# Kernel optimization log

Hardware: AMD Instinct MI355X
Metric: run time of the kernel (lower is better)

The kernel has to match this reference:

```python
import jax, jax.numpy as jnp
import numpy as np

B, C, T, F = 4, 2, 4224, 256
L = 256          # sequence_len (block size over time)
STRIDE = 128
H = 8            # num_heads
RF = L // 2      # receptive_field default


def setup_inputs() -> dict:
    key = jax.random.key(0)
    k0, k1, k2, k3, k4 = jax.random.split(key, 5)
    s = 0.05
    return {
        "x": jax.random.normal(k0, (B, C, T, F), dtype=jnp.float32),
        "w_in": jax.random.normal(k1, (3 * F, F), dtype=jnp.float32) * s,
        "b_in": jax.random.normal(k2, (3 * F,), dtype=jnp.float32) * s,
        "w_out": jax.random.normal(k3, (F, F), dtype=jnp.float32) * s,
        "b_out": jax.random.normal(k4, (F,), dtype=jnp.float32) * s,
    }


def reference(x, w_in, b_in, w_out, b_out):
    b, c, t, f = x.shape
    nb = (t - L) // STRIDE + 1              # num_blocks
    dh = f // H                              # head dim

    # --- UnfoldSpectrogram: (B,C,T,F) -> (B,C,nb,L,F) ---
    idx = jnp.arange(nb)[:, None] * STRIDE + jnp.arange(L)[None, :]  # (nb, L)
    blocks = x[:, :, idx, :]                 # (B,C,nb,L,F)

    # --- MultiheadAttention over flattened batch of blocks ---
    xb = blocks.reshape(b * c * nb, L, f)    # (N,L,F)
    qkv = xb @ w_in.T + b_in                 # (N,L,3F)
    q, k, v = jnp.split(qkv, 3, axis=-1)
    q = q.reshape(-1, L, H, dh)
    k = k.reshape(-1, L, H, dh)
    v = v.reshape(-1, L, H, dh)

    scale = 1.0 / np.sqrt(dh).astype(np.float32)
    scores = jnp.einsum("nihd,njhd->nhij", q, k) * scale  # (N,H,L,L)

    # Faithful to the original: the Longformer mask is a FLOAT 0/1 tensor that
    # torch's MultiheadAttention ADDS to the scores (band gets +1.0).
    di = jnp.arange(L)[:, None] - jnp.arange(L)[None, :]
    band = ((di >= 0) & (di < RF)).astype(scores.dtype)   # (L,L)
    scores = scores + band

    attn = jax.nn.softmax(scores, axis=-1)
    o = jnp.einsum("nhij,njhd->nihd", attn, v).reshape(-1, L, f)
    o = o @ w_out.T + b_out                  # (N,L,F)

    # --- FoldSpectrogram: overlap-add then normalize by overlap count ---
    ob = o.reshape(b, c, nb, L, f)
    y = jnp.zeros((b, c, t, f), dtype=o.dtype).at[:, :, idx, :].add(ob)
    cnt = jnp.zeros((t,), dtype=o.dtype).at[idx.reshape(-1)].add(1.0)
    return y / cnt[None, None, :, None]
```

## Files before the change

### kernel.cpp

```cpp
#include <hip/hip_runtime.h>

typedef unsigned short u16;
typedef unsigned int u32;
typedef __attribute__((ext_vector_type(8))) short bf16x8;
typedef __attribute__((ext_vector_type(4))) float f32x4;
typedef __attribute__((ext_vector_type(4))) u32 u32x4;
typedef __attribute__((ext_vector_type(2))) u32 u32x2;

__device__ __forceinline__ u16 f2bf(float f) {
  u32 u = __builtin_bit_cast(u32, f);
  return (u16)((u + 0x7FFFu + ((u >> 16) & 1u)) >> 16);
}
__device__ __forceinline__ float bf2f(u16 b) {
  return __builtin_bit_cast(float, (u32)b << 16);
}

__device__ __forceinline__ u32 cvtpk(float lo, float hi) {
  u32 r;
  asm("v_cvt_pk_bf16_f32 %0, %1, %2" : "=v"(r) : "v"(lo), "v"(hi));
  return r;
}

__device__ __forceinline__ float fexp2(float x) {
#if __has_builtin(__builtin_amdgcn_exp2f)
  return __builtin_amdgcn_exp2f(x);
#else
  return __expf(x * 0.6931471805599453f);
#endif
}

__device__ __forceinline__ void lds_async16(const void* g, void* l) {
  auto gp = reinterpret_cast<const __attribute__((address_space(1))) u32*>(
      reinterpret_cast<uintptr_t>(g));
  auto lp = reinterpret_cast<__attribute__((address_space(3))) u32*>(
      reinterpret_cast<uintptr_t>(l));
  __builtin_amdgcn_global_load_lds(gp, lp, 16, 0, 0);
}

__global__ void cvt2_kernel(const float* __restrict__ a, const float* __restrict__ b,
                            u16* __restrict__ oa, u16* __restrict__ ob, int na4, int nb4) {
  int i = blockIdx.x * 256 + threadIdx.x;
  const float* src;
  u16* dst;
  int idx;
  if (i < na4) {
    src = a; dst = oa; idx = i;
  } else {
    idx = i - na4;
    if (idx >= nb4) return;
    src = b; dst = ob;
  }
  f32x4 v = *(const f32x4*)(src + (size_t)idx * 4);
  u32x2 o;
  o[0] = (u32)f2bf(v[0]) | ((u32)f2bf(v[1]) << 16);
  o[1] = (u32)f2bf(v[2]) | ((u32)f2bf(v[3]) << 16);
  *(u32x2*)(dst + (size_t)idx * 4) = o;
}

template <bool OUT_BF16, bool A_F32>
__global__ __launch_bounds__(256) void gemm_bt_kernel(
    const void* __restrict__ A, const u16* __restrict__ B,
    const float* __restrict__ bias, void* __restrict__ C,
    int M, int N, int K) {
  __shared__ u16 sA[128 * 32];
  __shared__ u16 sB[128 * 32];
  const int tid = threadIdx.x;
  const int m0 = blockIdx.x * 128;
  const int n0 = blockIdx.y * 128;
  const int w = tid >> 6;
  const int lane = tid & 63;
  const int wr = (w >> 1) * 64;
  const int wc = (w & 1) * 64;
  const int lm = lane & 15;
  const int lk = (lane >> 4) * 8;

  f32x4 acc[4][4] = {};

  const int srow = tid >> 2;
  const int ssub = (tid & 3) * 8;
  const u16* Ag = (const u16*)A + (size_t)(m0 + srow) * K + ssub;
  const float* Agf = (const float*)A + (size_t)(m0 + srow) * K + ssub;
  const u16* Bg = B + (size_t)(n0 + srow) * K + ssub;
  const size_t rstep = (size_t)64 * K;

  for (int k0 = 0; k0 < K; k0 += 32) {
    f32x4 a00, a01, a10, a11;
    if constexpr (A_F32) {
      a00 = *(const f32x4*)(Agf + k0);
      a01 = *(const f32x4*)(Agf + k0 + 4);
      a10 = *(const f32x4*)(Agf + rstep + k0);
      a11 = *(const f32x4*)(Agf + rstep + k0 + 4);
    }
    __syncthreads();
    if constexpr (A_F32) {
      u32x4 w0, w1;
      w0[0] = cvtpk(a00[0], a00[1]); w0[1] = cvtpk(a00[2], a00[3]);
      w0[2] = cvtpk(a01[0], a01[1]); w0[3] = cvtpk(a01[2], a01[3]);
      w1[0] = cvtpk(a10[0], a10[1]); w1[1] = cvtpk(a10[2], a10[3]);
      w1[2] = cvtpk(a11[0], a11[1]); w1[3] = cvtpk(a11[2], a11[3]);
      *(u32x4*)&sA[tid * 8] = w0;
      *(u32x4*)&sA[2048 + tid * 8] = w1;
    } else {
      lds_async16(Ag + k0, &sA[tid * 8]);
      lds_async16(Ag + rstep + k0, &sA[2048 + tid * 8]);
    }
    lds_async16(Bg + k0, &sB[tid * 8]);
    lds_async16(Bg + rstep + k0, &sB[2048 + tid * 8]);
    __syncthreads();
    bf16x8 af[4], bfr[4];
#pragma unroll
    for (int i = 0; i < 4; ++i)
      af[i] = *(const bf16x8*)&sA[(wr + i * 16 + lm) * 32 + lk];
#pragma unroll
    for (int j = 0; j < 4; ++j)
      bfr[j] = *(const bf16x8*)&sB[(wc + j * 16 + lm) * 32 + lk];
#pragma unroll
    for (int i = 0; i < 4; ++i)
#pragma unroll
      for (int j = 0; j < 4; ++j)
        acc[i][j] = __builtin_amdgcn_mfma_f32_16x16x32_bf16(af[i], bfr[j], acc[i][j], 0, 0, 0);
  }

  const int r0 = (lane >> 4) * 4;
#pragma unroll
  for (int j = 0; j < 4; ++j) {
    const int n = n0 + wc + j * 16 + lm;
    const float bv = bias[n];
#pragma unroll
    for (int i = 0; i < 4; ++i) {
#pragma unroll
      for (int r = 0; r < 4; ++r) {
        const int m = m0 + wr + i * 16 + r0 + r;
        float v = acc[i][j][r] + bv;
        if (OUT_BF16)
          ((u16*)C)[(size_t)m * N + n] = f2bf(v);
        else
          ((float*)C)[(size_t)m * N + n] = v;
      }
    }
  }
}

__global__ __launch_bounds__(256, 2) void attn_kernel(const u16* __restrict__ qkv,
                                                      u16* __restrict__ o_ws) {
  __shared__ u16 sVt[32 * 264];
  __shared__ u16 sP[4 * 32 * 40];

  const int bid = blockIdx.x;
  const int n = bid >> 3;
  const int h = bid & 7;
  const int rowbase = (n >> 5) * 4224 + (n & 31) * 128;
  const int tid = threadIdx.x;
  const int w = tid >> 6;
  const int lane = tid & 63;
  const int lm = lane & 15;
  const int lg = lane >> 4;

#pragma unroll
  for (int it = 0; it < 4; ++it) {
    int c = it * 256 + tid;
    int row = c >> 2;
    int sub = (c & 3) * 8;
    int rsw = row ^ ((sub >> 3) << 4);
    const u16* gv = qkv + (size_t)(rowbase + row) * 768 + 512 + h * 32 + sub;
    u32x4 vv = *(const u32x4*)gv;
#pragma unroll
    for (int q = 0; q < 4; ++q) {
      sVt[(sub + 2 * q) * 264 + rsw] = (u16)(vv[q] & 0xFFFFu);
      sVt[(sub + 2 * q + 1) * 264 + rsw] = (u16)(vv[q] >> 16);
    }
  }

  bf16x8 qf[4];
#pragma unroll
  for (int rt = 0; rt < 4; ++rt) {
    int row = rowbase + w * 64 + rt * 16 + lm;
    qf[rt] = *(const bf16x8*)(qkv + (size_t)row * 768 + h * 32 + lg * 8);
  }

  const u16* kbase = qkv + (size_t)(rowbase + lm) * 768 + 256 + h * 32 + lg * 8;

  bf16x8 kfc[2];
#pragma unroll
  for (int ct = 0; ct < 2; ++ct)
    kfc[ct] = *(const bf16x8*)(kbase + (size_t)(ct * 16) * 768);

  __syncthreads();

  f32x4 oacc[4][2] = {};
  f32x4 lacc[4] = {};
  u16* myP = sP + w * (32 * 40);
  const float C1 = 0.25500035370494726f;
  const float C2 = 1.4426950408889634f;
  const int jq = lg * 4;
  const int D0w = w * 64;
  const bf16x8 onesb = {(short)0x3F80, (short)0x3F80, (short)0x3F80, (short)0x3F80,
                        (short)0x3F80, (short)0x3F80, (short)0x3F80, (short)0x3F80};

#pragma unroll 1
  for (int ch = 0; ch < 8; ++ch) {
    const int chn = (ch < 7) ? ch + 1 : 7;
    bf16x8 kfn[2], vf[2];
#pragma unroll
    for (int ct = 0; ct < 2; ++ct)
      kfn[ct] = *(const bf16x8*)(kbase + (size_t)(chn * 32 + ct * 16) * 768);
#pragma unroll
    for (int ctd = 0; ctd < 2; ++ctd) {
      int d = ctd * 16 + lm;
      vf[ctd] = *(const bf16x8*)&sVt[d * 264 + ((ch * 32 + lg * 8) ^ ((d >> 3) << 4))];
    }

#pragma unroll
    for (int hf = 0; hf < 2; ++hf) {
#pragma unroll
      for (int ct = 0; ct < 2; ++ct) {
#pragma unroll
        for (int rl = 0; rl < 2; ++rl) {
          const int rt = hf * 2 + rl;
          f32x4 s = __builtin_amdgcn_mfma_f32_16x16x32_bf16(kfc[ct], qf[rt], f32x4{0.f, 0.f, 0.f, 0.f}, 0, 0, 0);
          const int D0 = D0w + rt * 16 - (ch * 32 + ct * 16);
          float p0, p1, p2, p3;
          if (D0 >= 16 && D0 <= 112) {
            p0 = fexp2(__builtin_fmaf(s[0], C1, C2));
            p1 = fexp2(__builtin_fmaf(s[1], C1, C2));
            p2 = fexp2(__builtin_fmaf(s[2], C1, C2));
            p3 = fexp2(__builtin_fmaf(s[3], C1, C2));
          } else if (D0 == 0) {
            p0 = fexp2(__builtin_fmaf(s[0], C1, (lm >= jq + 0) ? C2 : 0.0f));
            p1 = fexp2(__builtin_fmaf(s[1], C1, (lm >= jq + 1) ? C2 : 0.0f));
            p2 = fexp2(__builtin_fmaf(s[2], C1, (lm >= jq + 2) ? C2 : 0.0f));
            p3 = fexp2(__builtin_fmaf(s[3], C1, (lm >= jq + 3) ? C2 : 0.0f));
          } else if (D0 == 128) {
            p0 = fexp2(__builtin_fmaf(s[0], C1, (lm < jq + 0) ? C2 : 0.0f));
            p1 = fexp2(__builtin_fmaf(s[1], C1, (lm < jq + 1) ? C2 : 0.0f));
            p2 = fexp2(__builtin_fmaf(s[2], C1, (lm < jq + 2) ? C2 : 0.0f));
            p3 = fexp2(__builtin_fmaf(s[3], C1, (lm < jq + 3) ? C2 : 0.0f));
          } else {
            p0 = fexp2(s[0] * C1);
            p1 = fexp2(s[1] * C1);
            p2 = fexp2(s[2] * C1);
            p3 = fexp2(s[3] * C1);
          }
          u32 a0, a1;
          asm("v_cvt_pk_bf16_f32 %0, %1, %2" : "=v"(a0) : "v"(p0), "v"(p1));
          asm("v_cvt_pk_bf16_f32 %0, %1, %2" : "=v"(a1) : "v"(p2), "v"(p3));
          u32x2 pk;
          pk[0] = a0;
          pk[1] = a1;
          *(u32x2*)&myP[(rl * 16 + lm) * 40 + ct * 16 + jq] = pk;
        }
      }
      bf16x8 pf[2];
#pragma unroll
      for (int rl = 0; rl < 2; ++rl)
        pf[rl] = *(const bf16x8*)&myP[(rl * 16 + lm) * 40 + lg * 8];
      __asm__ __volatile__("" ::: "memory");
      __builtin_amdgcn_s_setprio(1);
#pragma unroll
      for (int rl = 0; rl < 2; ++rl) {
        lacc[hf * 2 + rl] =
            __builtin_amdgcn_mfma_f32_16x16x32_bf16(pf[rl], onesb, lacc[hf * 2 + rl], 0, 0, 0);
#pragma unroll
        for (int ctd = 0; ctd < 2; ++ctd)
          oacc[hf * 2 + rl][ctd] =
              __builtin_amdgcn_mfma_f32_16x16x32_bf16(pf[rl], vf[ctd], oacc[hf * 2 + rl][ctd], 0, 0, 0);
      }
      __builtin_amdgcn_s_setprio(0);
    }
    kfc[0] = kfn[0];
    kfc[1] = kfn[1];
  }

#pragma unroll
  for (int rt = 0; rt < 4; ++rt) {
#pragma unroll
    for (int r = 0; r < 4; ++r) {
      float inv = 1.0f / lacc[rt][r];
      int i_g = w * 64 + rt * 16 + jq + r;
#pragma unroll
      for (int ctd = 0; ctd < 2; ++ctd) {
        float v = oacc[rt][ctd][r] * inv;
        u32 u = __builtin_bit_cast(u32, v) + 0x8000u;
        o_ws[((size_t)(n * 256 + i_g)) * 256 + h * 32 + ctd * 16 + lm] = (u16)(u >> 16);
      }
    }
  }
}

__global__ void combine_kernel(const u16* __restrict__ o_ws, u16* __restrict__ oc) {
  int gid = blockIdx.x * 256 + threadIdx.x;
  int m = gid >> 5;
  int f0 = (gid & 31) << 3;
  int bc = m / 4224;
  int t = m - bc * 4224;
  int i0 = t >> 7;
  float a[8] = {0.f, 0.f, 0.f, 0.f, 0.f, 0.f, 0.f, 0.f};
  if (i0 <= 31) {
    const u16* p = o_ws + ((size_t)((bc * 32 + i0) * 256 + (t - (i0 << 7)))) * 256 + f0;
    u32x4 v = *(const u32x4*)p;
#pragma unroll
    for (int q = 0; q < 4; ++q) {
      a[2 * q] += bf2f((u16)(v[q] & 0xFFFFu));
      a[2 * q + 1] += bf2f((u16)(v[q] >> 16));
    }
  }
  if (i0 >= 1) {
    int i1 = i0 - 1;
    const u16* p = o_ws + ((size_t)((bc * 32 + i1) * 256 + (t - (i1 << 7)))) * 256 + f0;
    u32x4 v = *(const u32x4*)p;
#pragma unroll
    for (int q = 0; q < 4; ++q) {
      a[2 * q] += bf2f((u16)(v[q] & 0xFFFFu));
      a[2 * q + 1] += bf2f((u16)(v[q] >> 16));
    }
  }
  float sc = (i0 >= 1 && i0 <= 31) ? 0.5f : 1.0f;
  u32x2 o;
  o[0] = (u32)f2bf(a[0] * sc) | ((u32)f2bf(a[1] * sc) << 16);
  o[1] = (u32)f2bf(a[2] * sc) | ((u32)f2bf(a[3] * sc) << 16);
  u32x2 o2;
  o2[0] = (u32)f2bf(a[4] * sc) | ((u32)f2bf(a[5] * sc) << 16);
  o2[1] = (u32)f2bf(a[6] * sc) | ((u32)f2bf(a[7] * sc) << 16);
  u16* dst = oc + (size_t)m * 256 + f0;
  *(u32x2*)dst = o;
  *(u32x2*)(dst + 4) = o2;
}

extern "C" void kernel_launch(void* const* d_in, const int* in_sizes, int n_in,
                              void* d_out, int out_size, void* d_ws, size_t ws_size,
                              hipStream_t stream) {
  const float* x = (const float*)d_in[0];
  const float* w_in = (const float*)d_in[1];
  const float* b_in = (const float*)d_in[2];
  const float* w_out = (const float*)d_in[3];
  const float* b_out = (const float*)d_in[4];
  float* y = (float*)d_out;
  char* ws = (char*)d_ws;

  u16* qkv = (u16*)(ws);
  u16* xbf = (u16*)(ws + 51904512);
  u16* ows = (u16*)(ws + 69206016);
  u16* winb = (u16*)(ws + 102760448);
  u16* woutb = (u16*)(ws + 103153664);

  cvt2_kernel<<<256, 256, 0, stream>>>(w_in, w_out, winb, woutb, 49152, 16384);

  gemm_bt_kernel<true, true><<<dim3(264, 6), 256, 0, stream>>>(x, winb, b_in, qkv, 33792, 768, 256);

  attn_kernel<<<2048, 256, 0, stream>>>(qkv, ows);

  combine_kernel<<<4224, 256, 0, stream>>>(ows, xbf);

  gemm_bt_kernel<false, false><<<dim3(264, 2), 256, 0, stream>>>(xbf, woutb, b_out, y, 33792, 256, 256);
}
```

Before: 180.0 us.

## Fuse overlap-add combine into output projection GEMM A-tile loading

Removes the separate combine kernel and folds the overlap-add of the two overlapping attention blocks into the A-operand staging of the output-projection GEMM. The 0.5 normalization moves after the GEMM as an fma with the bias, which is valid because the projection is linear. This removes a full bf16 write and reread of the combined activations plus one kernel launch. In exchange, A loads become synchronous register loads with add-and-convert work before each LDS store, rather than async copies. The sum is also rounded to bf16 before scaling, which slightly changes numerics.

```diff
diff --git a/kernel.cpp b/kernel.cpp
--- a/kernel.cpp
+++ b/kernel.cpp
@@ -136,6 +136,106 @@
           ((u16*)C)[(size_t)m * N + n] = f2bf(v);
         else
           ((float*)C)[(size_t)m * N + n] = v;
+      }
+    }
+  }
+}
+
+__global__ __launch_bounds__(256) void gemm2_fused_kernel(
+    const u16* __restrict__ ows, const u16* __restrict__ B,
+    const float* __restrict__ bias, float* __restrict__ C,
+    int M, int N, int K) {
+  __shared__ u16 sA[128 * 32];
+  __shared__ u16 sB[128 * 32];
+  const int tid = threadIdx.x;
+  const int x = blockIdx.x;
+  const int m0 = x * 128;
+  const int n0 = blockIdx.y * 128;
+  const int bc = x / 33;
+  const int ib = x - bc * 33;
+  const bool has0 = (ib <= 31);
+  const bool has1 = (ib >= 1);
+  const float sc = (has0 && has1) ? 0.5f : 1.0f;
+  const int w = tid >> 6;
+  const int lane = tid & 63;
+  const int wr = (w >> 1) * 64;
+  const int wc = (w & 1) * 64;
+  const int lm = lane & 15;
+  const int lk = (lane >> 4) * 8;
+
+  f32x4 acc[4][4] = {};
+
+  const int srow = tid >> 2;
+  const int ssub = (tid & 3) * 8;
+  const u16* A0 = ows + ((size_t)((bc * 32 + ib) * 256 + srow)) * 256 + ssub;
+  const u16* A1 = ows + ((size_t)((bc * 32 + ib - 1) * 256 + 128 + srow)) * 256 + ssub;
+  const size_t arstep = (size_t)64 * 256;
+  const u16* Bg = B + (size_t)(n0 + srow) * K + ssub;
+  const size_t rstep = (size_t)64 * K;
+
+  for (int k0 = 0; k0 < K; k0 += 32) {
+    u32x4 a00{}, a01{}, a10{}, a11{};
+    if (has0) {
+      a00 = *(const u32x4*)(A0 + k0);
+      a01 = *(const u32x4*)(A0 + arstep + k0);
+    }
+    if (has1) {
+      a10 = *(const u32x4*)(A1 + k0);
+      a11 = *(const u32x4*)(A1 + arstep + k0);
+    }
+    __syncthreads();
+    if (has0 && has1) {
+      u32x4 w0, w1;
+#pragma unroll
+      for (int q = 0; q < 4; ++q) {
+        float e0 = __builtin_bit_cast(float, a00[q] << 16) +
+                   __builtin_bit_cast(float, a10[q] << 16);
+        float o0 = __builtin_bit_cast(float, a00[q] & 0xFFFF0000u) +
+                   __builtin_bit_cast(float, a10[q] & 0xFFFF0000u);
+        w0[q] = cvtpk(e0, o0);
+        float e1 = __builtin_bit_cast(float, a01[q] << 16) +
+                   __builtin_bit_cast(float, a11[q] << 16);
+        float o1 = __builtin_bit_cast(float, a01[q] & 0xFFFF0000u) +
+                   __builtin_bit_cast(float, a11[q] & 0xFFFF0000u);
+        w1[q] = cvtpk(e1, o1);
+      }
+      *(u32x4*)&sA[tid * 8] = w0;
+      *(u32x4*)&sA[2048 + tid * 8] = w1;
+    } else if (has0) {
+      *(u32x4*)&sA[tid * 8] = a00;
+      *(u32x4*)&sA[2048 + tid * 8] = a01;
+    } else {
+      *(u32x4*)&sA[tid * 8] = a10;
+      *(u32x4*)&sA[2048 + tid * 8] = a11;
+    }
+    lds_async16(Bg + k0, &sB[tid * 8]);
+    lds_async16(Bg + rstep + k0, &sB[2048 + tid * 8]);
+    __syncthreads();
+    bf16x8 af[4], bfr[4];
+#pragma unroll
+    for (int i = 0; i < 4; ++i)
+      af[i] = *(const bf16x8*)&sA[(wr + i * 16 + lm) * 32 + lk];
+#pragma unroll
+    for (int j = 0; j < 4; ++j)
+      bfr[j] = *(const bf16x8*)&sB[(wc + j * 16 + lm) * 32 + lk];
+#pragma unroll
+    for (int i = 0; i < 4; ++i)
+#pragma unroll
+      for (int j = 0; j < 4; ++j)
+        acc[i][j] = __builtin_amdgcn_mfma_f32_16x16x32_bf16(af[i], bfr[j], acc[i][j], 0, 0, 0);
+  }
+
+  const int r0 = (lane >> 4) * 4;
+#pragma unroll
+  for (int j = 0; j < 4; ++j) {
+    const int n = n0 + wc + j * 16 + lm;
+    const float bv = bias[n];
+#pragma unroll
+    for (int i = 0; i < 4; ++i) {
+#pragma unroll
+      for (int r = 0; r < 4; ++r) {
+        const int m = m0 + wr + i * 16 + r0 + r;
+        C[(size_t)m * N + n] = __builtin_fmaf(sc, acc[i][j][r], bv);
       }
     }
   }
@@ -287,45 +387,6 @@
   }
 }
 
-__global__ void combine_kernel(const u16* __restrict__ o_ws, u16* __restrict__ oc) {
-  int gid = blockIdx.x * 256 + threadIdx.x;
-  int m = gid >> 5;
-  int f0 = (gid & 31) << 3;
-  int bc = m / 4224;
-  int t = m - bc * 4224;
-  int i0 = t >> 7;
-  float a[8] = {0.f, 0.f, 0.f, 0.f, 0.f, 0.f, 0.f, 0.f};
-  if (i0 <= 31) {
-    const u16* p = o_ws + ((size_t)((bc * 32 + i0) * 256 + (t - (i0 << 7)))) * 256 + f0;
-    u32x4 v = *(const u32x4*)p;
-#pragma unroll
-    for (int q = 0; q < 4; ++q) {
-      a[2 * q] += bf2f((u16)(v[q] & 0xFFFFu));
-      a[2 * q + 1] += bf2f((u16)(v[q] >> 16));
-    }
-  }
-  if (i0 >= 1) {
-    int i1 = i0 - 1;
-    const u16* p = o_ws + ((size_t)((bc * 32 + i1) * 256 + (t - (i1 << 7)))) * 256 + f0;
-    u32x4 v = *(const u32x4*)p;
-#pragma unroll
-    for (int q = 0; q < 4; ++q) {
-      a[2 * q] += bf2f((u16)(v[q] & 0xFFFFu));
-      a[2 * q + 1] += bf2f((u16)(v[q] >> 16));
-    }
-  }
-  float sc = (i0 >= 1 && i0 <= 31) ? 0.5f : 1.0f;
-  u32x2 o;
-  o[0] = (u32)f2bf(a[0] * sc) | ((u32)f2bf(a[1] * sc) << 16);
-  o[1] = (u32)f2bf(a[2] * sc) | ((u32)f2bf(a[3] * sc) << 16);
-  u32x2 o2;
-  o2[0] = (u32)f2bf(a[4] * sc) | ((u32)f2bf(a[5] * sc) << 16);
-  o2[1] = (u32)f2bf(a[6] * sc) | ((u32)f2bf(a[7] * sc) << 16);
-  u16* dst = oc + (size_t)m * 256 + f0;
-  *(u32x2*)dst = o;
-  *(u32x2*)(dst + 4) = o2;
-}
-
 extern "C" void kernel_launch(void* const* d_in, const int* in_sizes, int n_in,
                               void* d_out, int out_size, void* d_ws, size_t ws_size,
                               hipStream_t stream) {
@@ -338,7 +399,6 @@
   char* ws = (char*)d_ws;
 
   u16* qkv = (u16*)(ws);
-  u16* xbf = (u16*)(ws + 51904512);
   u16* ows = (u16*)(ws + 69206016);
   u16* winb = (u16*)(ws + 102760448);
   u16* woutb = (u16*)(ws + 103153664);
@@ -349,7 +409,5 @@
 
   attn_kernel<<<2048, 256, 0, stream>>>(qkv, ows);
 
-  combine_kernel<<<4224, 256, 0, stream>>>(ows, xbf);
-
-  gemm_bt_kernel<false, false><<<dim3(264, 2), 256, 0, stream>>>(xbf, woutb, b_out, y, 33792, 256, 256);
-}
+  gemm2_fused_kernel<<<dim3(264, 2), 256, 0, stream>>>(ows, woutb, b_out, y, 33792, 256, 256);
+}
```

After: 175.0 us. 2.8% less time.
